# Optimization experiments

Measured on AMD Instinct MI355X. Metric: run time of the kernel, lower is better.

## Reference

```python
import jax, jax.numpy as jnp
import numpy as np

N = 50000      # nodes
E = 800000     # edges
D_IN = 128
D_H = 128
D_OUT = 64


def _glorot(key, fan_in, fan_out):
    s = float(np.sqrt(6.0 / (fan_in + fan_out)))
    return jax.random.uniform(key, (fan_in, fan_out), jnp.float32, -s, s)


def setup_inputs() -> dict:
    key = jax.random.key(0)
    ks = jax.random.split(key, 8)
    x = jax.random.normal(ks[0], (N, D_IN), jnp.float32)
    edge_index = jax.random.randint(ks[1], (2, E), 0, N, dtype=jnp.int32)
    return {
        "x": x,
        "edge_index": edge_index,
        "W0": _glorot(ks[2], D_IN, D_H), "b0": jnp.zeros((D_H,), jnp.float32),
        "W1": _glorot(ks[3], D_H, D_H),  "b1": jnp.zeros((D_H,), jnp.float32),
        "W2": _glorot(ks[4], D_H, D_H),  "b2": jnp.zeros((D_H,), jnp.float32),
        "W_out": _glorot(ks[5], D_H, D_OUT), "b_out": jnp.zeros((D_OUT,), jnp.float32),
    }


def reference(x, edge_index, W0, b0, W1, b1, W2, b2, W_out, b_out):
    src = edge_index[0]
    dst = edge_index[1]
    # GCN normalization with self-loops: deg = in-degree(dst) + 1
    deg = jax.ops.segment_sum(jnp.ones((E,), x.dtype), dst, num_segments=N) + 1.0
    dinv = jax.lax.rsqrt(deg)                       # [N]
    edge_coef = (dinv[src] * dinv[dst])[:, None]    # [E,1]
    self_coef = (dinv * dinv)[:, None]              # [N,1]

    def gcn_conv(h, W, b):
        h = h @ W                                            # [N,F]
        agg = jax.ops.segment_sum(h[src] * edge_coef, dst, num_segments=N)
        agg = agg + h * self_coef                            # self-loop term
        return agg + b

    h = x
    for W, b in ((W0, b0), (W1, b1), (W2, b2)):
        h_in = h
        h = jax.nn.relu(gcn_conv(h, W, b))  # eval mode: dropout is identity
        if h.shape == h_in.shape:
            h = h + h_in
    return h @ W_out + b_out
```

## Files before the change

kernel.cpp:

```cpp
#include <hip/hip_runtime.h>

#define N_NODES 50000
#define N_EDGES 800000

static inline int cdiv(int a, int b) { return (a + b - 1) / b; }

typedef __attribute__((ext_vector_type(8))) short s8vec;
typedef __attribute__((ext_vector_type(4))) float f32x4;

__device__ inline ushort f2b(float f) {
    uint u = __float_as_uint(f);
    uint r = (u + 0x7fffu + ((u >> 16) & 1u)) >> 16;
    return (ushort)r;
}
__device__ inline float b2f_lo(uint v) { return __uint_as_float(v << 16); }
__device__ inline float b2f_hi(uint v) { return __uint_as_float(v & 0xffff0000u); }

__device__ inline void acc8(float* acc, uint4 v, float c) {
    acc[0] += b2f_lo(v.x) * c; acc[1] += b2f_hi(v.x) * c;
    acc[2] += b2f_lo(v.y) * c; acc[3] += b2f_hi(v.y) * c;
    acc[4] += b2f_lo(v.z) * c; acc[5] += b2f_hi(v.z) * c;
    acc[6] += b2f_lo(v.w) * c; acc[7] += b2f_hi(v.w) * c;
}


__global__ __launch_bounds__(256) void k_prep(int* cnt,
                                              const float* __restrict__ W0, const float* __restrict__ W1,
                                              const float* __restrict__ W2, const float* __restrict__ Wo,
                                              ushort* Wt0, ushort* Wt1, ushort* Wt2, ushort* Wto) {
    int b = blockIdx.x;
    if (b < 196) {
        int i = b * 256 + threadIdx.x;
        if (i < N_NODES) cnt[i] = 0;
        return;
    }
    int i = (b - 196) * 256 + threadIdx.x;
    if (i < 16384) {
        int nn = i >> 7, k = i & 127;
        Wt0[i] = f2b(W0[k * 128 + nn]);
    } else if (i < 32768) {
        int j = i - 16384; int nn = j >> 7, k = j & 127;
        Wt1[j] = f2b(W1[k * 128 + nn]);
    } else if (i < 49152) {
        int j = i - 32768; int nn = j >> 7, k = j & 127;
        Wt2[j] = f2b(W2[k * 128 + nn]);
    } else if (i < 57344) {
        int j = i - 49152; int nn = j >> 7, k = j & 127;
        Wto[j] = f2b(Wo[k * 64 + nn]);
    }
}

__global__ __launch_bounds__(256) void k_count(const int* __restrict__ dst, int* cnt, int e) {
    int i = blockIdx.x * 256 + threadIdx.x;
    if (i < e) atomicAdd(&cnt[dst[i]], 1);
}


__global__ __launch_bounds__(512) void k_block_sum(const int* __restrict__ cnt, int* bsum, int n) {
    __shared__ int sh[512];
    int i = blockIdx.x * 512 + threadIdx.x;
    sh[threadIdx.x] = (i < n) ? cnt[i] : 0;
    __syncthreads();
    for (int off = 256; off > 0; off >>= 1) {
        if (threadIdx.x < off) sh[threadIdx.x] += sh[threadIdx.x + off];
        __syncthreads();
    }
    if (threadIdx.x == 0) bsum[blockIdx.x] = sh[0];
}

__global__ __launch_bounds__(128) void k_scan_bsum(const int* __restrict__ bsum, int* boff,
                                                   int nb, int* rowptr, int n, int e) {
    __shared__ int sh[128];
    int t = threadIdx.x;
    int v = (t < nb) ? bsum[t] : 0;
    sh[t] = v;
    __syncthreads();
    for (int off = 1; off < 128; off <<= 1) {
        int add = (t >= off) ? sh[t - off] : 0;
        __syncthreads();
        sh[t] += add;
        __syncthreads();
    }
    if (t < nb) boff[t] = sh[t] - v;
    if (t == 0) rowptr[n] = e;
}

__global__ __launch_bounds__(512) void k_scan_block(const int* __restrict__ cnt,
                                                    const int* __restrict__ boff,
                                                    int* rowptr, int* cursor, float* dinv, int n) {
    __shared__ int sh[512];
    int t = threadIdx.x;
    int i = blockIdx.x * 512 + t;
    int v = (i < n) ? cnt[i] : 0;
    sh[t] = v;
    __syncthreads();
    for (int off = 1; off < 512; off <<= 1) {
        int add = (t >= off) ? sh[t - off] : 0;
        __syncthreads();
        sh[t] += add;
        __syncthreads();
    }
    if (i < n) {
        rowptr[i] = sh[t] - v + boff[blockIdx.x];
        cursor[i] = 0;
        dinv[i] = rsqrtf((float)v + 1.0f);
    }
}


template <int NCOL, bool IN_F32, bool OUT_F32>
__device__ inline void mm_body(const void* __restrict__ Av, const ushort* __restrict__ Wt,
                               const float* __restrict__ bias, void* __restrict__ Cv,
                               int n, int bid) {
    constexpr int NT = NCOL / 16;
    int wave = threadIdx.x >> 6;
    int lane = threadIdx.x & 63;
    int quad = lane >> 4;
    int lm = lane & 15;
    int row0 = bid * 128 + wave * 32;

    int rA0 = row0 + lm;      if (rA0 > n - 1) rA0 = n - 1;
    int rA1 = row0 + 16 + lm; if (rA1 > n - 1) rA1 = n - 1;

    f32x4 acc[2][NT];
#pragma unroll
    for (int r = 0; r < 2; r++)
#pragma unroll
        for (int t = 0; t < NT; t++) acc[r][t] = (f32x4){0.f, 0.f, 0.f, 0.f};

    for (int kc = 0; kc < 128; kc += 32) {
        s8vec af[2];
        if (IN_F32) {
            const float* A = (const float*)Av;
#pragma unroll
            for (int r = 0; r < 2; r++) {
                const float* p = A + (size_t)(r ? rA1 : rA0) * 128 + quad * 8 + kc;
                float4 a = *(const float4*)p, b = *(const float4*)(p + 4);
                s8vec v;
                v[0] = (short)f2b(a.x); v[1] = (short)f2b(a.y);
                v[2] = (short)f2b(a.z); v[3] = (short)f2b(a.w);
                v[4] = (short)f2b(b.x); v[5] = (short)f2b(b.y);
                v[6] = (short)f2b(b.z); v[7] = (short)f2b(b.w);
                af[r] = v;
            }
        } else {
            const ushort* A = (const ushort*)Av;
            af[0] = *(const s8vec*)(A + (size_t)rA0 * 128 + quad * 8 + kc);
            af[1] = *(const s8vec*)(A + (size_t)rA1 * 128 + quad * 8 + kc);
        }
#pragma unroll
        for (int t = 0; t < NT; t++) {
            s8vec bf = *(const s8vec*)(Wt + (size_t)(t * 16 + lm) * 128 + kc + quad * 8);
            acc[0][t] = __builtin_amdgcn_mfma_f32_16x16x32_bf16(af[0], bf, acc[0][t], 0, 0, 0);
            acc[1][t] = __builtin_amdgcn_mfma_f32_16x16x32_bf16(af[1], bf, acc[1][t], 0, 0, 0);
        }
    }

#pragma unroll
    for (int r = 0; r < 2; r++) {
#pragma unroll
        for (int t = 0; t < NT; t++) {
            int col = t * 16 + lm;
            float bv = OUT_F32 ? bias[col] : 0.f;
#pragma unroll
            for (int i = 0; i < 4; i++) {
                int rr = row0 + r * 16 + quad * 4 + i;
                if (rr < n) {
                    if (OUT_F32)
                        ((float*)Cv)[(size_t)rr * NCOL + col] = acc[r][t][i] + bv;
                    else
                        ((ushort*)Cv)[(size_t)rr * 128 + col] = f2b(acc[r][t][i]);
                }
            }
        }
    }
}

template <int NCOL, bool IN_F32, bool OUT_F32>
__global__ __launch_bounds__(256) void k_mm(const void* __restrict__ Av,
                                            const ushort* __restrict__ Wt,
                                            const float* __restrict__ bias,
                                            void* __restrict__ Cv, int n) {
    mm_body<NCOL, IN_F32, OUT_F32>(Av, Wt, bias, Cv, n, blockIdx.x);
}

__global__ __launch_bounds__(256) void k_mm0_fill(const void* __restrict__ Av,
                                                  const ushort* __restrict__ Wt,
                                                  void* __restrict__ Cv, int n, int mmblocks,
                                                  const int* __restrict__ src, const int* __restrict__ dst,
                                                  const float* __restrict__ dinv,
                                                  const int* __restrict__ rowptr, int* cursor,
                                                  uint2* ed, int e) {
    if ((int)blockIdx.x >= mmblocks) {
        int i = ((int)blockIdx.x - mmblocks) * 256 + threadIdx.x;
        if (i < e) {
            int d = dst[i], s = src[i];
            int pos = rowptr[d] + atomicAdd(&cursor[d], 1);
            float c = dinv[s] * dinv[d];
            ed[pos] = make_uint2((uint)s, __float_as_uint(c));
        }
        return;
    }
    mm_body<128, true, false>(Av, Wt, nullptr, Cv, n, blockIdx.x);
}


template <bool RES_F32>
__global__ __launch_bounds__(256) void k_gatherb(const uint4* __restrict__ T4,
                                                 const int* __restrict__ rowptr,
                                                 const uint2* __restrict__ ed,
                                                 const float* __restrict__ dinv,
                                                 const float* __restrict__ bias,
                                                 const void* __restrict__ resv,
                                                 uint4* __restrict__ out4, int n) {
    int node = blockIdx.x * 16 + (threadIdx.x >> 4);
    if (node >= n) return;
    int ql = threadIdx.x & 15;
    int qb = threadIdx.x & 48;

    float acc[8] = {0.f, 0.f, 0.f, 0.f, 0.f, 0.f, 0.f, 0.f};
    int beg = rowptr[node], end = rowptr[node + 1];

    for (int base = beg; base < end; base += 16) {
        int m = end - base; if (m > 16) m = 16;
        uint2 em = make_uint2(0u, 0u);
        if (base + ql < end) em = ed[base + ql];
        int j = 0;
        for (; j + 4 <= m; j += 4) {
            int s0 = __shfl((int)em.x, qb + j);
            int s1 = __shfl((int)em.x, qb + j + 1);
            int s2 = __shfl((int)em.x, qb + j + 2);
            int s3 = __shfl((int)em.x, qb + j + 3);
            float c0 = __uint_as_float((uint)__shfl((int)em.y, qb + j));
            float c1 = __uint_as_float((uint)__shfl((int)em.y, qb + j + 1));
            float c2 = __uint_as_float((uint)__shfl((int)em.y, qb + j + 2));
            float c3 = __uint_as_float((uint)__shfl((int)em.y, qb + j + 3));
            uint4 v0 = T4[(size_t)s0 * 16 + ql];
            uint4 v1 = T4[(size_t)s1 * 16 + ql];
            uint4 v2 = T4[(size_t)s2 * 16 + ql];
            uint4 v3 = T4[(size_t)s3 * 16 + ql];
            acc8(acc, v0, c0); acc8(acc, v1, c1);
            acc8(acc, v2, c2); acc8(acc, v3, c3);
        }
        for (; j < m; j++) {
            int s = __shfl((int)em.x, qb + j);
            float c = __uint_as_float((uint)__shfl((int)em.y, qb + j));
            uint4 v = T4[(size_t)s * 16 + ql];
            acc8(acc, v, c);
        }
    }

    float di = dinv[node];
    float sc = di * di;
    uint4 vs = T4[(size_t)node * 16 + ql];
    float self[8] = {b2f_lo(vs.x), b2f_hi(vs.x), b2f_lo(vs.y), b2f_hi(vs.y),
                     b2f_lo(vs.z), b2f_hi(vs.z), b2f_lo(vs.w), b2f_hi(vs.w)};
    float4 bv0 = ((const float4*)bias)[ql * 2];
    float4 bv1 = ((const float4*)bias)[ql * 2 + 1];
    float bb[8] = {bv0.x, bv0.y, bv0.z, bv0.w, bv1.x, bv1.y, bv1.z, bv1.w};

    float r[8];
    if (RES_F32) {
        float4 r0 = ((const float4*)resv)[(size_t)node * 32 + ql * 2];
        float4 r1 = ((const float4*)resv)[(size_t)node * 32 + ql * 2 + 1];
        r[0] = r0.x; r[1] = r0.y; r[2] = r0.z; r[3] = r0.w;
        r[4] = r1.x; r[5] = r1.y; r[6] = r1.z; r[7] = r1.w;
    } else {
        uint4 rv = ((const uint4*)resv)[(size_t)node * 16 + ql];
        r[0] = b2f_lo(rv.x); r[1] = b2f_hi(rv.x); r[2] = b2f_lo(rv.y); r[3] = b2f_hi(rv.y);
        r[4] = b2f_lo(rv.z); r[5] = b2f_hi(rv.z); r[6] = b2f_lo(rv.w); r[7] = b2f_hi(rv.w);
    }

    float o[8];
#pragma unroll
    for (int i = 0; i < 8; i++)
        o[i] = fmaxf(acc[i] + self[i] * sc + bb[i], 0.f) + r[i];

    uint4 ov;
    ov.x = (uint)f2b(o[0]) | ((uint)f2b(o[1]) << 16);
    ov.y = (uint)f2b(o[2]) | ((uint)f2b(o[3]) << 16);
    ov.z = (uint)f2b(o[4]) | ((uint)f2b(o[5]) << 16);
    ov.w = (uint)f2b(o[6]) | ((uint)f2b(o[7]) << 16);
    out4[(size_t)node * 16 + ql] = ov;
}


extern "C" void kernel_launch(void* const* d_in, const int* in_sizes, int n_in,
                              void* d_out, int out_size, void* d_ws, size_t ws_size,
                              hipStream_t stream) {
    const float* x  = (const float*)d_in[0];
    const int* eidx = (const int*)d_in[1];
    const float* W0 = (const float*)d_in[2];
    const float* b0 = (const float*)d_in[3];
    const float* W1 = (const float*)d_in[4];
    const float* b1 = (const float*)d_in[5];
    const float* W2 = (const float*)d_in[6];
    const float* b2 = (const float*)d_in[7];
    const float* Wo = (const float*)d_in[8];
    const float* bo = (const float*)d_in[9];
    float* out = (float*)d_out;

    const int N = N_NODES, E = N_EDGES;
    const int* srcI = eidx;
    const int* dstI = eidx + E;
    const int NB512 = cdiv(N, 512);

    char* ws = (char*)d_ws;
    auto alloc = [&](size_t bytes) { char* p = ws; ws += (bytes + 255) / 256 * 256; return p; };
    int*    cnt    = (int*)alloc((size_t)N * 4);
    int*    cursor = (int*)alloc((size_t)N * 4);
    int*    rowptr = (int*)alloc((size_t)(N + 1) * 4);
    int*    bsum   = (int*)alloc((size_t)NB512 * 4);
    int*    boff   = (int*)alloc((size_t)NB512 * 4);
    float*  dinv   = (float*)alloc((size_t)N * 4);
    uint2*  ed     = (uint2*)alloc((size_t)E * 8);
    ushort* tmpb   = (ushort*)alloc((size_t)N * 128 * 2);
    ushort* hAb    = (ushort*)alloc((size_t)N * 128 * 2);
    ushort* hBb    = (ushort*)alloc((size_t)N * 128 * 2);
    ushort* Wt0    = (ushort*)alloc(128 * 128 * 2);
    ushort* Wt1    = (ushort*)alloc(128 * 128 * 2);
    ushort* Wt2    = (ushort*)alloc(128 * 128 * 2);
    ushort* Wto    = (ushort*)alloc(64 * 128 * 2);

    dim3 b256(256), b512(512);

    const int mmGrid = cdiv(N, 128);
    const int fillGrid = cdiv(E, 256);
    const int gGrid = cdiv(N, 16);

    k_prep<<<196 + 224, b256, 0, stream>>>(cnt, W0, W1, W2, Wo, Wt0, Wt1, Wt2, Wto);
    k_count<<<cdiv(E, 256), b256, 0, stream>>>(dstI, cnt, E);
    k_block_sum<<<NB512, b512, 0, stream>>>(cnt, bsum, N);
    k_scan_bsum<<<1, 128, 0, stream>>>(bsum, boff, NB512, rowptr, N, E);
    k_scan_block<<<NB512, b512, 0, stream>>>(cnt, boff, rowptr, cursor, dinv, N);

    k_mm0_fill<<<mmGrid + fillGrid, b256, 0, stream>>>(x, Wt0, tmpb, N, mmGrid,
                                                       srcI, dstI, dinv, rowptr, cursor, ed, E);
    k_gatherb<true><<<gGrid, b256, 0, stream>>>((const uint4*)tmpb, rowptr, ed, dinv, b0, x, (uint4*)hAb, N);

    k_mm<128, false, false><<<mmGrid, b256, 0, stream>>>(hAb, Wt1, nullptr, tmpb, N);
    k_gatherb<false><<<gGrid, b256, 0, stream>>>((const uint4*)tmpb, rowptr, ed, dinv, b1, hAb, (uint4*)hBb, N);

    k_mm<128, false, false><<<mmGrid, b256, 0, stream>>>(hBb, Wt2, nullptr, tmpb, N);
    k_gatherb<false><<<gGrid, b256, 0, stream>>>((const uint4*)tmpb, rowptr, ed, dinv, b2, hBb, (uint4*)hAb, N);

    k_mm<64, false, true><<<mmGrid, b256, 0, stream>>>(hAb, Wto, bo, out, N);
}
```

Before: 312.1 us.

## Fold symmetric GCN normalization into matmul epilogue and shrink edge list

The source-side dinv scaling moves into the matmul epilogue and the destination-side scaling into the gather epilogue, so the CSR edge list holds only 4-byte source indices instead of (index, coefficient) pairs. This halves edge-list traffic in each gather and removes a shuffle and an FMA per edge. The three-kernel scan is replaced by a single-block 1024-thread scan that initializes the cursor to rowptr, so the fill step needs one atomic and no rowptr read. The fill kernel also processes four edges per thread. The catch is that the single-block scan is serial over 50k counts, and bf16 rounding of the prescaled values differs slightly from before.

```diff
diff --git a/kernel.cpp b/kernel.cpp
--- a/kernel.cpp
+++ b/kernel.cpp
@@ -16,11 +16,11 @@
 __device__ inline float b2f_lo(uint v) { return __uint_as_float(v << 16); }
 __device__ inline float b2f_hi(uint v) { return __uint_as_float(v & 0xffff0000u); }
 
-__device__ inline void acc8(float* acc, uint4 v, float c) {
-    acc[0] += b2f_lo(v.x) * c; acc[1] += b2f_hi(v.x) * c;
-    acc[2] += b2f_lo(v.y) * c; acc[3] += b2f_hi(v.y) * c;
-    acc[4] += b2f_lo(v.z) * c; acc[5] += b2f_hi(v.z) * c;
-    acc[6] += b2f_lo(v.w) * c; acc[7] += b2f_hi(v.w) * c;
+__device__ inline void add8(float* acc, uint4 v) {
+    acc[0] += b2f_lo(v.x); acc[1] += b2f_hi(v.x);
+    acc[2] += b2f_lo(v.y); acc[3] += b2f_hi(v.y);
+    acc[4] += b2f_lo(v.z); acc[5] += b2f_hi(v.z);
+    acc[6] += b2f_lo(v.w); acc[7] += b2f_hi(v.w);
 }
 
 
@@ -56,62 +56,62 @@
 }
 
 
-__global__ __launch_bounds__(512) void k_block_sum(const int* __restrict__ cnt, int* bsum, int n) {
-    __shared__ int sh[512];
-    int i = blockIdx.x * 512 + threadIdx.x;
-    sh[threadIdx.x] = (i < n) ? cnt[i] : 0;
+__global__ __launch_bounds__(1024) void k_scan(const int* __restrict__ cnt,
+                                               int* __restrict__ rowptr, int* __restrict__ cursor,
+                                               float* __restrict__ dinv, int n, int e) {
+    constexpr int PER = 52;
+    __shared__ int sh[1024];
+    int t = threadIdx.x;
+    int base = t * PER;
+
+    int v[PER];
+#pragma unroll
+    for (int j = 0; j < PER; j += 4) {
+        int4 q;
+        if (base + j + 3 < n) {
+            q = *(const int4*)(cnt + base + j);
+        } else {
+            q.x = (base + j     < n) ? cnt[base + j]     : 0;
+            q.y = (base + j + 1 < n) ? cnt[base + j + 1] : 0;
+            q.z = (base + j + 2 < n) ? cnt[base + j + 2] : 0;
+            q.w = (base + j + 3 < n) ? cnt[base + j + 3] : 0;
+        }
+        v[j] = q.x; v[j + 1] = q.y; v[j + 2] = q.z; v[j + 3] = q.w;
+    }
+
+    int sum = 0;
+#pragma unroll
+    for (int j = 0; j < PER; j++) { int x = v[j]; v[j] = sum; sum += x; }
+
+    sh[t] = sum;
     __syncthreads();
-    for (int off = 256; off > 0; off >>= 1) {
-        if (threadIdx.x < off) sh[threadIdx.x] += sh[threadIdx.x + off];
-        __syncthreads();
-    }
-    if (threadIdx.x == 0) bsum[blockIdx.x] = sh[0];
-}
-
-__global__ __launch_bounds__(128) void k_scan_bsum(const int* __restrict__ bsum, int* boff,
-                                                   int nb, int* rowptr, int n, int e) {
-    __shared__ int sh[128];
-    int t = threadIdx.x;
-    int v = (t < nb) ? bsum[t] : 0;
-    sh[t] = v;
-    __syncthreads();
-    for (int off = 1; off < 128; off <<= 1) {
+    for (int off = 1; off < 1024; off <<= 1) {
         int add = (t >= off) ? sh[t - off] : 0;
         __syncthreads();
         sh[t] += add;
         __syncthreads();
     }
-    if (t < nb) boff[t] = sh[t] - v;
+    int tb = sh[t] - sum;
+
+#pragma unroll
+    for (int j = 0; j < PER; j++) {
+        int i = base + j;
+        if (i < n) {
+            int rp = tb + v[j];
+            rowptr[i] = rp;
+            cursor[i] = rp;
+            int cj = ((j + 1 < PER) ? v[j + 1] : sum) - v[j];
+            dinv[i] = rsqrtf((float)cj + 1.0f);
+        }
+    }
     if (t == 0) rowptr[n] = e;
 }
 
-__global__ __launch_bounds__(512) void k_scan_block(const int* __restrict__ cnt,
-                                                    const int* __restrict__ boff,
-                                                    int* rowptr, int* cursor, float* dinv, int n) {
-    __shared__ int sh[512];
-    int t = threadIdx.x;
-    int i = blockIdx.x * 512 + t;
-    int v = (i < n) ? cnt[i] : 0;
-    sh[t] = v;
-    __syncthreads();
-    for (int off = 1; off < 512; off <<= 1) {
-        int add = (t >= off) ? sh[t - off] : 0;
-        __syncthreads();
-        sh[t] += add;
-        __syncthreads();
-    }
-    if (i < n) {
-        rowptr[i] = sh[t] - v + boff[blockIdx.x];
-        cursor[i] = 0;
-        dinv[i] = rsqrtf((float)v + 1.0f);
-    }
-}
-
-
-template <int NCOL, bool IN_F32, bool OUT_F32>
+
+template <int NCOL, bool IN_F32, bool OUT_F32, bool SCALE>
 __device__ inline void mm_body(const void* __restrict__ Av, const ushort* __restrict__ Wt,
-                               const float* __restrict__ bias, void* __restrict__ Cv,
-                               int n, int bid) {
+                               const float* __restrict__ bias, const float* __restrict__ dinv,
+                               void* __restrict__ Cv, int n, int bid) {
     constexpr int NT = NCOL / 16;
     int wave = threadIdx.x >> 6;
     int lane = threadIdx.x & 63;
@@ -159,56 +159,60 @@
 #pragma unroll
     for (int r = 0; r < 2; r++) {
 #pragma unroll
-        for (int t = 0; t < NT; t++) {
-            int col = t * 16 + lm;
-            float bv = OUT_F32 ? bias[col] : 0.f;
-#pragma unroll
-            for (int i = 0; i < 4; i++) {
-                int rr = row0 + r * 16 + quad * 4 + i;
-                if (rr < n) {
+        for (int i = 0; i < 4; i++) {
+            int rr = row0 + r * 16 + quad * 4 + i;
+            if (rr < n) {
+                float dv = SCALE ? dinv[rr] : 1.0f;
+#pragma unroll
+                for (int t = 0; t < NT; t++) {
+                    int col = t * 16 + lm;
                     if (OUT_F32)
-                        ((float*)Cv)[(size_t)rr * NCOL + col] = acc[r][t][i] + bv;
+                        ((float*)Cv)[(size_t)rr * NCOL + col] = acc[r][t][i] + bias[col];
                     else
-                        ((ushort*)Cv)[(size_t)rr * 128 + col] = f2b(acc[r][t][i]);
+                        ((ushort*)Cv)[(size_t)rr * 128 + col] =
+                            f2b(SCALE ? acc[r][t][i] * dv : acc[r][t][i]);
                 }
             }
         }
     }
 }
 
-template <int NCOL, bool IN_F32, bool OUT_F32>
+template <int NCOL, bool IN_F32, bool OUT_F32, bool SCALE>
 __global__ __launch_bounds__(256) void k_mm(const void* __restrict__ Av,
                                             const ushort* __restrict__ Wt,
                                             const float* __restrict__ bias,
+                                            const float* __restrict__ dinv,
                                             void* __restrict__ Cv, int n) {
-    mm_body<NCOL, IN_F32, OUT_F32>(Av, Wt, bias, Cv, n, blockIdx.x);
+    mm_body<NCOL, IN_F32, OUT_F32, SCALE>(Av, Wt, bias, dinv, Cv, n, blockIdx.x);
 }
 
 __global__ __launch_bounds__(256) void k_mm0_fill(const void* __restrict__ Av,
                                                   const ushort* __restrict__ Wt,
+                                                  const float* __restrict__ dinv,
                                                   void* __restrict__ Cv, int n, int mmblocks,
                                                   const int* __restrict__ src, const int* __restrict__ dst,
-                                                  const float* __restrict__ dinv,
-                                                  const int* __restrict__ rowptr, int* cursor,
-                                                  uint2* ed, int e) {
+                                                  int* cursor, uint* ed, int e) {
     if ((int)blockIdx.x >= mmblocks) {
-        int i = ((int)blockIdx.x - mmblocks) * 256 + threadIdx.x;
-        if (i < e) {
-            int d = dst[i], s = src[i];
-            int pos = rowptr[d] + atomicAdd(&cursor[d], 1);
-            float c = dinv[s] * dinv[d];
-            ed[pos] = make_uint2((uint)s, __float_as_uint(c));
+        int base = ((int)blockIdx.x - mmblocks) * 1024 + threadIdx.x;
+#pragma unroll
+        for (int k = 0; k < 4; k++) {
+            int i = base + k * 256;
+            if (i < e) {
+                int d = dst[i], s = src[i];
+                int pos = atomicAdd(&cursor[d], 1);
+                ed[pos] = (uint)s;
+            }
         }
         return;
     }
-    mm_body<128, true, false>(Av, Wt, nullptr, Cv, n, blockIdx.x);
+    mm_body<128, true, false, true>(Av, Wt, nullptr, dinv, Cv, n, blockIdx.x);
 }
 
 
 template <bool RES_F32>
 __global__ __launch_bounds__(256) void k_gatherb(const uint4* __restrict__ T4,
                                                  const int* __restrict__ rowptr,
-                                                 const uint2* __restrict__ ed,
+                                                 const uint* __restrict__ ed,
                                                  const float* __restrict__ dinv,
                                                  const float* __restrict__ bias,
                                                  const void* __restrict__ resv,
@@ -223,38 +227,31 @@
 
     for (int base = beg; base < end; base += 16) {
         int m = end - base; if (m > 16) m = 16;
-        uint2 em = make_uint2(0u, 0u);
-        if (base + ql < end) em = ed[base + ql];
+        int idx = base + ql; if (idx > end - 1) idx = end - 1;
+        uint em = ed[idx];
         int j = 0;
         for (; j + 4 <= m; j += 4) {
-            int s0 = __shfl((int)em.x, qb + j);
-            int s1 = __shfl((int)em.x, qb + j + 1);
-            int s2 = __shfl((int)em.x, qb + j + 2);
-            int s3 = __shfl((int)em.x, qb + j + 3);
-            float c0 = __uint_as_float((uint)__shfl((int)em.y, qb + j));
-            float c1 = __uint_as_float((uint)__shfl((int)em.y, qb + j + 1));
-            float c2 = __uint_as_float((uint)__shfl((int)em.y, qb + j + 2));
-            float c3 = __uint_as_float((uint)__shfl((int)em.y, qb + j + 3));
+            int s0 = __shfl((int)em, qb + j);
+            int s1 = __shfl((int)em, qb + j + 1);
+            int s2 = __shfl((int)em, qb + j + 2);
+            int s3 = __shfl((int)em, qb + j + 3);
             uint4 v0 = T4[(size_t)s0 * 16 + ql];
             uint4 v1 = T4[(size_t)s1 * 16 + ql];
             uint4 v2 = T4[(size_t)s2 * 16 + ql];
             uint4 v3 = T4[(size_t)s3 * 16 + ql];
-            acc8(acc, v0, c0); acc8(acc, v1, c1);
-            acc8(acc, v2, c2); acc8(acc, v3, c3);
+            add8(acc, v0); add8(acc, v1); add8(acc, v2); add8(acc, v3);
         }
         for (; j < m; j++) {
-            int s = __shfl((int)em.x, qb + j);
-            float c = __uint_as_float((uint)__shfl((int)em.y, qb + j));
+            int s = __shfl((int)em, qb + j);
             uint4 v = T4[(size_t)s * 16 + ql];
-            acc8(acc, v, c);
-        }
-    }
+            add8(acc, v);
+        }
+    }
+
+    uint4 vs = T4[(size_t)node * 16 + ql];
+    add8(acc, vs);
 
     float di = dinv[node];
-    float sc = di * di;
-    uint4 vs = T4[(size_t)node * 16 + ql];
-    float self[8] = {b2f_lo(vs.x), b2f_hi(vs.x), b2f_lo(vs.y), b2f_hi(vs.y),
-                     b2f_lo(vs.z), b2f_hi(vs.z), b2f_lo(vs.w), b2f_hi(vs.w)};
     float4 bv0 = ((const float4*)bias)[ql * 2];
     float4 bv1 = ((const float4*)bias)[ql * 2 + 1];
     float bb[8] = {bv0.x, bv0.y, bv0.z, bv0.w, bv1.x, bv1.y, bv1.z, bv1.w};
@@ -274,7 +271,7 @@
     float o[8];
 #pragma unroll
     for (int i = 0; i < 8; i++)
-        o[i] = fmaxf(acc[i] + self[i] * sc + bb[i], 0.f) + r[i];
+        o[i] = fmaxf(acc[i] * di + bb[i], 0.f) + r[i];
 
     uint4 ov;
     ov.x = (uint)f2b(o[0]) | ((uint)f2b(o[1]) << 16);
@@ -303,17 +300,14 @@
     const int N = N_NODES, E = N_EDGES;
     const int* srcI = eidx;
     const int* dstI = eidx + E;
-    const int NB512 = cdiv(N, 512);
 
     char* ws = (char*)d_ws;
     auto alloc = [&](size_t bytes) { char* p = ws; ws += (bytes + 255) / 256 * 256; return p; };
     int*    cnt    = (int*)alloc((size_t)N * 4);
     int*    cursor = (int*)alloc((size_t)N * 4);
     int*    rowptr = (int*)alloc((size_t)(N + 1) * 4);
-    int*    bsum   = (int*)alloc((size_t)NB512 * 4);
-    int*    boff   = (int*)alloc((size_t)NB512 * 4);
     float*  dinv   = (float*)alloc((size_t)N * 4);
-    uint2*  ed     = (uint2*)alloc((size_t)E * 8);
+    uint*   ed     = (uint*)alloc((size_t)E * 4);
     ushort* tmpb   = (ushort*)alloc((size_t)N * 128 * 2);
     ushort* hAb    = (ushort*)alloc((size_t)N * 128 * 2);
     ushort* hBb    = (ushort*)alloc((size_t)N * 128 * 2);
@@ -322,27 +316,25 @@
     ushort* Wt2    = (ushort*)alloc(128 * 128 * 2);
     ushort* Wto    = (ushort*)alloc(64 * 128 * 2);
 
-    dim3 b256(256), b512(512);
-
-    const int mmGrid = cdiv(N, 128);
-    const int fillGrid = cdiv(E, 256);
-    const int gGrid = cdiv(N, 16);
+    dim3 b256(256);
+
+    const int mmGrid   = cdiv(N, 128);
+    const int fillGrid = cdiv(E, 1024);
+    const int gGrid    = cdiv(N, 16);
 
     k_prep<<<196 + 224, b256, 0, stream>>>(cnt, W0, W1, W2, Wo, Wt0, Wt1, Wt2, Wto);
     k_count<<<cdiv(E, 256), b256, 0, stream>>>(dstI, cnt, E);
-    k_block_sum<<<NB512, b512, 0, stream>>>(cnt, bsum, N);
-    k_scan_bsum<<<1, 128, 0, stream>>>(bsum, boff, NB512, rowptr, N, E);
-    k_scan_block<<<NB512, b512, 0, stream>>>(cnt, boff, rowptr, cursor, dinv, N);
-
-    k_mm0_fill<<<mmGrid + fillGrid, b256, 0, stream>>>(x, Wt0, tmpb, N, mmGrid,
-                                                       srcI, dstI, dinv, rowptr, cursor, ed, E);
+    k_scan<<<1, 1024, 0, stream>>>(cnt, rowptr, cursor, dinv, N, E);
+
+    k_mm0_fill<<<mmGrid + fillGrid, b256, 0, stream>>>(x, Wt0, dinv, tmpb, N, mmGrid,
+                                                       srcI, dstI, cursor, ed, E);
     k_gatherb<true><<<gGrid, b256, 0, stream>>>((const uint4*)tmpb, rowptr, ed, dinv, b0, x, (uint4*)hAb, N);
 
-    k_mm<128, false, false><<<mmGrid, b256, 0, stream>>>(hAb, Wt1, nullptr, tmpb, N);
+    k_mm<128, false, false, true><<<mmGrid, b256, 0, stream>>>(hAb, Wt1, nullptr, dinv, tmpb, N);
     k_gatherb<false><<<gGrid, b256, 0, stream>>>((const uint4*)tmpb, rowptr, ed, dinv, b1, hAb, (uint4*)hBb, N);
 
-    k_mm<128, false, false><<<mmGrid, b256, 0, stream>>>(hBb, Wt2, nullptr, tmpb, N);
+    k_mm<128, false, false, true><<<mmGrid, b256, 0, stream>>>(hBb, Wt2, nullptr, dinv, tmpb, N);
     k_gatherb<false><<<gGrid, b256, 0, stream>>>((const uint4*)tmpb, rowptr, ed, dinv, b2, hBb, (uint4*)hAb, N);
 
-    k_mm<64, false, true><<<mmGrid, b256, 0, stream>>>(hAb, Wto, bo, out, N);
-}
+    k_mm<64, false, true, false><<<mmGrid, b256, 0, stream>>>(hAb, Wto, bo, dinv, out, N);
+}
```

Result: slower. 389.2 us (+24.7%).
